# Kernel tuning notes

Measured on AMD Instinct MI355X. Metric: run time of the kernel, lower is better.

## Reference

```python
import jax, jax.numpy as jnp
import numpy as np

IMAGE_SIZE = 256
NEAR = 0.1
FAR = 100.0
EPS = 1e-3
BACKGROUND = jnp.array([0.0, 0.0, 0.0], dtype=jnp.float32)
CHUNK = 64  # faces processed per scan step (keeps [B,CHUNK,3,P] intermediate ~100MB)


def setup_inputs() -> dict:
    key = jax.random.key(0)
    k1, k2, k3, k4 = jax.random.split(key, 4)
    B, F, T = 2, 4096, 4
    # small triangles in NDC with z in (near, far)
    centers = jax.random.uniform(k1, (B, F, 1, 2), minval=-1.0, maxval=1.0)
    offsets = 0.15 * jax.random.normal(k2, (B, F, 3, 2))
    xy = centers + offsets
    z = jax.random.uniform(k3, (B, F, 1, 1), minval=1.0, maxval=20.0) \
        + 0.1 * jax.random.normal(k4, (B, F, 3, 1))
    faces = jnp.concatenate([xy, z], axis=-1).astype(jnp.float32)  # [B,F,3,3]
    textures = jax.random.uniform(jax.random.fold_in(key, 7), (B, F, T, T, T, 3),
                                  dtype=jnp.float32)
    return {"faces": faces, "textures": textures}


def _pixel_grid(is_):
    c = (2.0 * jnp.arange(is_, dtype=jnp.float32) + 1.0 - is_) / is_
    # kernel iterates rows top->bottom with y flipped (y up in NDC)
    yp, xp = jnp.meshgrid(-c, c, indexing="ij")  # [H,W]
    return xp.reshape(-1), yp.reshape(-1)  # [P]


def _raster_chunk(fchunk, xp, yp, near, far):
    # fchunk: [B,C,3verts,3coords]; xp,yp: [P]
    x = fchunk[..., 0]
    y = fchunk[..., 1]
    z = fchunk[..., 2]  # [B,C,3]
    x0, x1, x2 = x[..., 0:1], x[..., 1:2], x[..., 2:3]
    y0, y1, y2 = y[..., 0:1], y[..., 1:2], y[..., 2:3]

    # inside test: pixel on the CCW side of all 3 edges (back faces culled)
    def edge(ya, xa, yb, xb):
        return (yp - ya) * (xb - xa) - (xp - xa) * (yb - ya)  # [B,C,P]
    inside = (edge(y0, x0, y1, x1) >= 0) & (edge(y1, x1, y2, x2) >= 0) \
             & (edge(y2, x2, y0, x0) >= 0)

    # inverse of [[x0,y0,1],[x1,y1,1],[x2,y2,1]] via adjugate (as in CUDA kernel)
    x0s, x1s, x2s = x[..., 0], x[..., 1], x[..., 2]
    y0s, y1s, y2s = y[..., 0], y[..., 1], y[..., 2]
    det = x2s * (y0s - y1s) + x0s * (y1s - y2s) + x1s * (y2s - y0s)
    det = jnp.where(det >= 0, jnp.maximum(det, 1e-10), jnp.minimum(det, -1e-10))
    inv = jnp.stack([
        jnp.stack([y1s - y2s, x2s - x1s, x1s * y2s - x2s * y1s], -1),
        jnp.stack([y2s - y0s, x0s - x2s, x2s * y0s - x0s * y2s], -1),
        jnp.stack([y0s - y1s, x1s - x0s, x0s * y1s - x1s * y0s], -1),
    ], -2) / det[..., None, None]  # [B,C,3,3]

    # barycentric weights per pixel: [B,C,3,P]
    w = inv[..., 0, None] * xp + inv[..., 1, None] * yp + inv[..., 2, None]
    w = jnp.clip(w, 0.0, 1.0)
    w = w / jnp.maximum(w.sum(axis=2, keepdims=True), 1e-10)

    # perspective-correct depth: 1/zp = sum_k w_k / z_k
    inv_zp = (w / z[..., None]).sum(axis=2)  # [B,C,P]
    zp = 1.0 / jnp.maximum(inv_zp, 1e-10)
    valid = inside & (zp > near) & (zp < far)
    zp = jnp.where(valid, zp, far)
    return zp, jnp.moveaxis(w, 2, 3)  # zp:[B,C,P], w:[B,C,P,3]


def _rasterize_maps(faces, image_size, near, far):
    B, F = faces.shape[:2]
    P = image_size * image_size
    xp, yp = _pixel_grid(image_size)
    n_chunks = F // CHUNK
    fch = faces.reshape(B, n_chunks, CHUNK, 3, 3).transpose(1, 0, 2, 3, 4)
    ids = jnp.arange(F, dtype=jnp.int32).reshape(n_chunks, CHUNK)
    init = (jnp.full((B, P), far, jnp.float32),        # best depth (z-buffer)
            jnp.full((B, P), -1, jnp.int32),            # best face index
            jnp.zeros((B, P, 3), jnp.float32))          # best barycentric weights

    def step(carry, inp):
        bz, bf, bw = carry
        fchunk, idc = inp
        zp, w = _raster_chunk(fchunk, xp, yp, near, far)
        am = jnp.argmin(zp, axis=1)  # [B,P] nearest face within chunk
        zmin = jnp.take_along_axis(zp, am[:, None, :], axis=1)[:, 0]          # [B,P]
        wsel = jnp.take_along_axis(w, am[:, None, :, None], axis=1)[:, 0]     # [B,P,3]
        fsel = idc[am]                                                        # [B,P]
        upd = zmin < bz
        return (jnp.where(upd, zmin, bz),
                jnp.where(upd, fsel, bf),
                jnp.where(upd[..., None], wsel, bw)), None

    (bz, bf, bw), _ = jax.lax.scan(jax.checkpoint(step), init, (fch, ids))
    return bf, bw, bz  # face_index_map, weight_map, depth_map (flat pixels)


def _forward(faces, textures):
    B, F = faces.shape[:2]
    T = textures.shape[2]
    is_ = IMAGE_SIZE
    P = is_ * is_
    fidx, w, zp = _rasterize_maps(faces, is_, NEAR, FAR)
    mask = fidx >= 0
    fi = jnp.maximum(fidx, 0)

    # per-pixel vertex depths of hit face: [B,P,3]
    faces_z = faces[..., 2]
    fz = jax.vmap(lambda a, i: a[i])(faces_z, fi)

    # texture cube coords with perspective correction (as in CUDA kernel)
    tif = jnp.clip(w * (T - 1) * (zp[..., None] / fz), 0.0, T - 1 - EPS)
    lo = jnp.floor(tif).astype(jnp.int32)
    frac = tif - lo

    tex_flat = textures.reshape(B, F, T * T * T, 3)
    rgb = jnp.zeros((B, P, 3), jnp.float32)
    for pn in range(8):  # trilinear blend over 8 cube corners
        bits = [(pn >> k) & 1 for k in range(3)]
        idx = lo + jnp.array(bits, jnp.int32)
        wc = jnp.ones_like(frac[..., 0])
        for k in range(3):
            wc = wc * (frac[..., k] if bits[k] else (1.0 - frac[..., k]))
        lin = (idx[..., 0] * T + idx[..., 1]) * T + idx[..., 2]
        texel = jax.vmap(lambda tf, f, l: tf[f, l])(tex_flat, fi, lin)  # [B,P,3]
        rgb = rgb + wc[..., None] * texel

    rgb = jnp.where(mask[..., None], rgb, BACKGROUND)
    alpha = mask.astype(jnp.float32)
    return (rgb.reshape(B, is_, is_, 3),
            alpha.reshape(B, is_, is_),
            zp.reshape(B, is_, is_))


def reference(faces, textures):
    return _forward(faces, textures)
```

## Files before the change

kernel.cpp:

```cpp
#include <hip/hip_runtime.h>

#define IS 256
#define FNUM 4096
#define BATCH 2
#define NSPLIT 16
#define FSPLIT (FNUM / NSPLIT)
#define FAR_ 100.0f
#define NEAR_ 0.1f


__global__ __launch_bounds__(256, 8) void raster_kernel(
    const float* __restrict__ faces, unsigned int* __restrict__ keys)
{
#pragma clang fp contract(off)
  __shared__ float rec[256 * 12];
  __shared__ int cnt[4];

  const int tid = threadIdx.x;
  const int wid = tid >> 6, lane = tid & 63;
  const int z = blockIdx.z;
  const int b = z >> 4;
  const int split = z & 15;

  const int qx = tid & 15, qy = tid >> 4;
  const int col0 = blockIdx.x * 32 + qx * 2;
  const int row0 = blockIdx.y * 32 + qy * 2;

  const float xpA = (2.0f * (float)col0 + 1.0f - 256.0f) * (1.0f / 256.0f);
  const float xpB = (2.0f * (float)(col0 + 1) + 1.0f - 256.0f) * (1.0f / 256.0f);
  const float ypA = -((2.0f * (float)row0 + 1.0f - 256.0f) * (1.0f / 256.0f));
  const float ypB = -((2.0f * (float)(row0 + 1) + 1.0f - 256.0f) * (1.0f / 256.0f));

  const float txmin = (2.0f * (float)(blockIdx.x * 32) + 1.0f - 256.0f) * (1.0f / 256.0f) - 1e-3f;
  const float txmax = (2.0f * (float)(blockIdx.x * 32 + 31) + 1.0f - 256.0f) * (1.0f / 256.0f) + 1e-3f;
  const float tymax = -((2.0f * (float)(blockIdx.y * 32) + 1.0f - 256.0f) * (1.0f / 256.0f)) + 1e-3f;
  const float tymin = -((2.0f * (float)(blockIdx.y * 32 + 31) + 1.0f - 256.0f) * (1.0f / 256.0f)) - 1e-3f;

  const int f = split * FSPLIT + tid;
  const float* fp = faces + ((size_t)b * FNUM + f) * 9;
  const float x0 = fp[0], y0 = fp[1], z0 = fp[2];
  const float x1 = fp[3], y1 = fp[4], z1 = fp[5];
  const float x2 = fp[6], y2 = fp[7], z2 = fp[8];

  const float det = x2 * (y0 - y1) + x0 * (y1 - y2) + x1 * (y2 - y0);
  const float minx = fminf(fminf(x0, x1), x2), maxx = fmaxf(fmaxf(x0, x1), x2);
  const float miny = fminf(fminf(y0, y1), y2), maxy = fmaxf(fmaxf(y0, y1), y2);
  const bool keep = (det >= -1e-5f) &&
                    (minx <= txmax) && (maxx >= txmin) &&
                    (miny <= tymax) && (maxy >= tymin);

  const unsigned long long m = __ballot(keep);
  if (lane == 0) cnt[wid] = __popcll(m);
  __syncthreads();
  const int total = cnt[0] + cnt[1] + cnt[2] + cnt[3];
  if (keep) {
    int base = 0;
    for (int w = 0; w < wid; ++w) base += cnt[w];
    const int pos = base + __popcll(m & ((1ull << lane) - 1ull));
    const float cd = (det >= 0.0f) ? fmaxf(det, 1e-10f) : fminf(det, -1e-10f);
    const float rdet = __builtin_amdgcn_rcpf(cd);
    const float u0 = __builtin_amdgcn_rcpf(z0) * rdet;
    const float u1 = __builtin_amdgcn_rcpf(z1) * rdet;
    const float u2 = __builtin_amdgcn_rcpf(z2) * rdet;
    float4* r4 = (float4*)&rec[pos * 12];
    r4[0] = make_float4(x0, y0, x1, y1);
    r4[1] = make_float4(x2, y2, u0, u1);
    r4[2] = make_float4(u2, __int_as_float(f), 0.0f, 0.0f);
  }
  __syncthreads();

  unsigned int kAA = ~0u, kAB = ~0u, kBA = ~0u, kBB = ~0u;
  for (int i = 0; i < total; ++i) {
    const float4 r0 = ((const float4*)rec)[i * 3 + 0];
    const float4 r1 = ((const float4*)rec)[i * 3 + 1];
    const float4 r2 = ((const float4*)rec)[i * 3 + 2];
    const float fx0 = r0.x, fy0 = r0.y, fx1 = r0.z, fy1 = r0.w;
    const float fx2 = r1.x, fy2 = r1.y, u0 = r1.z, u1 = r1.w;
    const float u2 = r2.x;
    const unsigned int fid = (unsigned int)__float_as_int(r2.y);

    const float t01x = fx1 - fx0, t01y = fy1 - fy0;
    const float t12x = fx2 - fx1, t12y = fy2 - fy1;
    const float t20x = fx0 - fx2, t20y = fy0 - fy2;

    const float a01A = (ypA - fy0) * t01x, a01B = (ypB - fy0) * t01x;
    const float b01A = (xpA - fx0) * t01y, b01B = (xpB - fx0) * t01y;
    const float a12A = (ypA - fy1) * t12x, a12B = (ypB - fy1) * t12x;
    const float b12A = (xpA - fx1) * t12y, b12B = (xpB - fx1) * t12y;
    const float a20A = (ypA - fy2) * t20x, a20B = (ypB - fy2) * t20x;
    const float b20A = (xpA - fx2) * t20y, b20B = (xpB - fx2) * t20y;

#define PX(KK, AR, AC)                                                        \
    {                                                                         \
      const float e01 = a01##AR - b01##AC;                                    \
      const float e12 = a12##AR - b12##AC;                                    \
      const float e20 = a20##AR - b20##AC;                                    \
      const bool inside = fminf(fminf(e01, e12), e20) >= 0.0f;                \
      const float izp = fmaf(e12, u0, fmaf(e20, u1, e01 * u2));               \
      const bool valid = inside && (izp > 0.01f) && (izp < 10.0f);            \
      const unsigned int key =                                                \
          valid ? ((~__float_as_uint(izp)) & 0xFFFFF000u) | fid : ~0u;        \
      KK = (key < KK) ? key : KK;                                             \
    }
    PX(kAA, A, A) PX(kAB, A, B) PX(kBA, B, A) PX(kBB, B, B)
#undef PX
  }

  const int pbase = b * 65536 + row0 * 256 + col0;
  if (kAA != ~0u) atomicMin(&keys[pbase], kAA);
  if (kAB != ~0u) atomicMin(&keys[pbase + 1], kAB);
  if (kBA != ~0u) atomicMin(&keys[pbase + 256], kBA);
  if (kBB != ~0u) atomicMin(&keys[pbase + 257], kBB);
}

struct __attribute__((packed, aligned(4))) F6 { float v[6]; };
struct __attribute__((packed, aligned(4))) F9 { float v[9]; };

__global__ __launch_bounds__(256) void resolve_kernel(
    const float* __restrict__ faces, const float* __restrict__ tex,
    const unsigned int* __restrict__ keys,
    float* __restrict__ out_rgb, float* __restrict__ out_alpha,
    float* __restrict__ out_z)
{
#pragma clang fp contract(off)
  const int p = blockIdx.x * 256 + threadIdx.x;
  const int b = p >> 16;
  const int pi = p & 65535;
  const int row = pi >> 8, col = pi & 255;

  const unsigned int key = keys[p];
  if (key == ~0u) {
    out_rgb[(size_t)p * 3 + 0] = 0.0f;
    out_rgb[(size_t)p * 3 + 1] = 0.0f;
    out_rgb[(size_t)p * 3 + 2] = 0.0f;
    out_alpha[p] = 0.0f;
    out_z[p] = FAR_;
    return;
  }

  const int fid = (int)(key & 0xFFFu);
  const float xp = (2.0f * (float)col + 1.0f - 256.0f) * (1.0f / 256.0f);
  const float yp = -((2.0f * (float)row + 1.0f - 256.0f) * (1.0f / 256.0f));

  const F9 fdat = *(const F9*)(faces + ((size_t)b * FNUM + fid) * 9);
  const float x0 = fdat.v[0], y0 = fdat.v[1], z0 = fdat.v[2];
  const float x1 = fdat.v[3], y1 = fdat.v[4], z1 = fdat.v[5];
  const float x2 = fdat.v[6], y2 = fdat.v[7], z2 = fdat.v[8];

  const float det = x2 * (y0 - y1) + x0 * (y1 - y2) + x1 * (y2 - y0);
  const float cd = (det >= 0.0f) ? fmaxf(det, 1e-10f) : fminf(det, -1e-10f);
  const float rdet = __builtin_amdgcn_rcpf(cd);
  const float rz0 = __builtin_amdgcn_rcpf(z0);
  const float rz1 = __builtin_amdgcn_rcpf(z1);
  const float rz2 = __builtin_amdgcn_rcpf(z2);

  const float e01 = (yp - y0) * (x1 - x0) - (xp - x0) * (y1 - y0);
  const float e12 = (yp - y1) * (x2 - x1) - (xp - x1) * (y2 - y1);
  const float e20 = (yp - y2) * (x0 - x2) - (xp - x2) * (y0 - y2);

  float c0 = fminf(fmaxf(e12 * rdet, 0.0f), 1.0f);
  float c1 = fminf(fmaxf(e20 * rdet, 0.0f), 1.0f);
  float c2 = fminf(fmaxf(e01 * rdet, 0.0f), 1.0f);
  const float s = fmaxf((c0 + c1) + c2, 1e-10f);
  const float rs = __builtin_amdgcn_rcpf(s);
  const float w0 = c0 * rs, w1 = c1 * rs, w2 = c2 * rs;
  const float izp = (w0 * rz0 + w1 * rz1) + w2 * rz2;
  const float zp = __builtin_amdgcn_rcpf(fmaxf(izp, 1e-10f));

  const float t0 = fminf(fmaxf((w0 * 3.0f) * (zp * rz0), 0.0f), 2.999f);
  const float t1 = fminf(fmaxf((w1 * 3.0f) * (zp * rz1), 0.0f), 2.999f);
  const float t2 = fminf(fmaxf((w2 * 3.0f) * (zp * rz2), 0.0f), 2.999f);
  const float l0 = floorf(t0), l1 = floorf(t1), l2 = floorf(t2);
  const int i0 = (int)l0, i1 = (int)l1, i2 = (int)l2;
  const float fr0 = t0 - l0, fr1 = t1 - l1, fr2 = t2 - l2;
  const float g0 = 1.0f - fr0, g1 = 1.0f - fr1, g2 = 1.0f - fr2;

  const float* tb = tex + ((size_t)b * FNUM + fid) * 192;
  float rr = 0.f, rg = 0.f, rb = 0.f;
#pragma unroll
  for (int pn = 0; pn < 4; ++pn) {
    const int b0 = pn & 1, b1 = (pn >> 1) & 1;
    const float w01 = (b0 ? fr0 : g0) * (b1 ? fr1 : g1);
    const float wz0 = w01 * g2, wz1 = w01 * fr2;
    const int lin0 = ((i0 + b0) * 4 + (i1 + b1)) * 4 + i2;
    const F6 t6 = *(const F6*)(tb + lin0 * 3);
    rr = rr + wz0 * t6.v[0] + wz1 * t6.v[3];
    rg = rg + wz0 * t6.v[1] + wz1 * t6.v[4];
    rb = rb + wz0 * t6.v[2] + wz1 * t6.v[5];
  }

  out_rgb[(size_t)p * 3 + 0] = rr;
  out_rgb[(size_t)p * 3 + 1] = rg;
  out_rgb[(size_t)p * 3 + 2] = rb;
  out_alpha[p] = 1.0f;
  out_z[p] = zp;
}

extern "C" void kernel_launch(void* const* d_in, const int* in_sizes, int n_in,
                              void* d_out, int out_size, void* d_ws, size_t ws_size,
                              hipStream_t stream) {
  const float* faces = (const float*)d_in[0];
  const float* tex   = (const float*)d_in[1];
  float* out = (float*)d_out;
  float* out_rgb   = out;
  float* out_alpha = out + 393216;
  float* out_z     = out + 393216 + 131072;

  unsigned int* keys = (unsigned int*)d_ws;
  hipMemsetAsync(keys, 0xFF, (size_t)BATCH * IS * IS * sizeof(unsigned int), stream);

  dim3 gridA(IS / 32, IS / 32, BATCH * NSPLIT);
  hipLaunchKernelGGL(raster_kernel, gridA, dim3(256), 0, stream, faces, keys);

  dim3 gridC((BATCH * IS * IS) / 256, 1, 1);
  hipLaunchKernelGGL(resolve_kernel, gridC, dim3(256), 0, stream,
                     faces, tex, keys, out_rgb, out_alpha, out_z);
}
```

Baseline: 75.50 us.

## Fuse resolve pass into raster kernel via last-block-per-tile ticket

Removes the separate resolve kernel. Each raster block increments a per-tile ticket counter, and the last of the split blocks for a tile shades that tile's pixels, reading keys with atomic loads. This saves one kernel launch and the round trip through the global key buffer. In exchange it adds a second memset for the tickets and concentrates the shading on only one block per tile. It also relies on atomics for cross-block visibility without an explicit fence.

```diff
diff --git a/kernel.cpp b/kernel.cpp
--- a/kernel.cpp
+++ b/kernel.cpp
@@ -7,14 +7,19 @@
 #define FSPLIT (FNUM / NSPLIT)
 #define FAR_ 100.0f
 #define NEAR_ 0.1f
+#define NTILE 64
 
 
 __global__ __launch_bounds__(256, 8) void raster_kernel(
-    const float* __restrict__ faces, unsigned int* __restrict__ keys)
+    const float* __restrict__ faces, const float* __restrict__ tex,
+    unsigned int* __restrict__ keys, unsigned int* __restrict__ tickets,
+    float* __restrict__ out_rgb, float* __restrict__ out_alpha,
+    float* __restrict__ out_z)
 {
 #pragma clang fp contract(off)
   __shared__ float rec[256 * 12];
   __shared__ int cnt[4];
+  __shared__ int lastflag;
 
   const int tid = threadIdx.x;
   const int wid = tid >> 6, lane = tid & 63;
@@ -36,38 +41,40 @@
   const float tymax = -((2.0f * (float)(blockIdx.y * 32) + 1.0f - 256.0f) * (1.0f / 256.0f)) + 1e-3f;
   const float tymin = -((2.0f * (float)(blockIdx.y * 32 + 31) + 1.0f - 256.0f) * (1.0f / 256.0f)) - 1e-3f;
 
-  const int f = split * FSPLIT + tid;
-  const float* fp = faces + ((size_t)b * FNUM + f) * 9;
-  const float x0 = fp[0], y0 = fp[1], z0 = fp[2];
-  const float x1 = fp[3], y1 = fp[4], z1 = fp[5];
-  const float x2 = fp[6], y2 = fp[7], z2 = fp[8];
-
-  const float det = x2 * (y0 - y1) + x0 * (y1 - y2) + x1 * (y2 - y0);
-  const float minx = fminf(fminf(x0, x1), x2), maxx = fmaxf(fmaxf(x0, x1), x2);
-  const float miny = fminf(fminf(y0, y1), y2), maxy = fmaxf(fmaxf(y0, y1), y2);
-  const bool keep = (det >= -1e-5f) &&
-                    (minx <= txmax) && (maxx >= txmin) &&
-                    (miny <= tymax) && (maxy >= tymin);
-
-  const unsigned long long m = __ballot(keep);
-  if (lane == 0) cnt[wid] = __popcll(m);
+  {
+    const int f = split * FSPLIT + tid;
+    const float* fp = faces + ((size_t)b * FNUM + f) * 9;
+    const float x0 = fp[0], y0 = fp[1], z0 = fp[2];
+    const float x1 = fp[3], y1 = fp[4], z1 = fp[5];
+    const float x2 = fp[6], y2 = fp[7], z2 = fp[8];
+
+    const float det = x2 * (y0 - y1) + x0 * (y1 - y2) + x1 * (y2 - y0);
+    const float minx = fminf(fminf(x0, x1), x2), maxx = fmaxf(fmaxf(x0, x1), x2);
+    const float miny = fminf(fminf(y0, y1), y2), maxy = fmaxf(fmaxf(y0, y1), y2);
+    const bool keep = (det >= -1e-5f) &&
+                      (minx <= txmax) && (maxx >= txmin) &&
+                      (miny <= tymax) && (maxy >= tymin);
+
+    const unsigned long long m = __ballot(keep);
+    if (lane == 0) cnt[wid] = __popcll(m);
+    __syncthreads();
+    if (keep) {
+      int base = 0;
+      for (int w = 0; w < wid; ++w) base += cnt[w];
+      const int pos = base + __popcll(m & ((1ull << lane) - 1ull));
+      const float cd = (det >= 0.0f) ? fmaxf(det, 1e-10f) : fminf(det, -1e-10f);
+      const float rdet = __builtin_amdgcn_rcpf(cd);
+      const float u0 = __builtin_amdgcn_rcpf(z0) * rdet;
+      const float u1 = __builtin_amdgcn_rcpf(z1) * rdet;
+      const float u2 = __builtin_amdgcn_rcpf(z2) * rdet;
+      float4* r4 = (float4*)&rec[pos * 12];
+      r4[0] = make_float4(x0, y0, x1, y1);
+      r4[1] = make_float4(x2, y2, u0, u1);
+      r4[2] = make_float4(u2, __int_as_float(f), 0.0f, 0.0f);
+    }
+  }
   __syncthreads();
   const int total = cnt[0] + cnt[1] + cnt[2] + cnt[3];
-  if (keep) {
-    int base = 0;
-    for (int w = 0; w < wid; ++w) base += cnt[w];
-    const int pos = base + __popcll(m & ((1ull << lane) - 1ull));
-    const float cd = (det >= 0.0f) ? fmaxf(det, 1e-10f) : fminf(det, -1e-10f);
-    const float rdet = __builtin_amdgcn_rcpf(cd);
-    const float u0 = __builtin_amdgcn_rcpf(z0) * rdet;
-    const float u1 = __builtin_amdgcn_rcpf(z1) * rdet;
-    const float u2 = __builtin_amdgcn_rcpf(z2) * rdet;
-    float4* r4 = (float4*)&rec[pos * 12];
-    r4[0] = make_float4(x0, y0, x1, y1);
-    r4[1] = make_float4(x2, y2, u0, u1);
-    r4[2] = make_float4(u2, __int_as_float(f), 0.0f, 0.0f);
-  }
-  __syncthreads();
 
   unsigned int kAA = ~0u, kAB = ~0u, kBA = ~0u, kBB = ~0u;
   for (int i = 0; i < total; ++i) {
@@ -111,89 +118,89 @@
   if (kAB != ~0u) atomicMin(&keys[pbase + 1], kAB);
   if (kBA != ~0u) atomicMin(&keys[pbase + 256], kBA);
   if (kBB != ~0u) atomicMin(&keys[pbase + 257], kBB);
-}
-
-struct __attribute__((packed, aligned(4))) F6 { float v[6]; };
-struct __attribute__((packed, aligned(4))) F9 { float v[9]; };
-
-__global__ __launch_bounds__(256) void resolve_kernel(
-    const float* __restrict__ faces, const float* __restrict__ tex,
-    const unsigned int* __restrict__ keys,
-    float* __restrict__ out_rgb, float* __restrict__ out_alpha,
-    float* __restrict__ out_z)
-{
-#pragma clang fp contract(off)
-  const int p = blockIdx.x * 256 + threadIdx.x;
-  const int b = p >> 16;
-  const int pi = p & 65535;
-  const int row = pi >> 8, col = pi & 255;
-
-  const unsigned int key = keys[p];
-  if (key == ~0u) {
-    out_rgb[(size_t)p * 3 + 0] = 0.0f;
-    out_rgb[(size_t)p * 3 + 1] = 0.0f;
-    out_rgb[(size_t)p * 3 + 2] = 0.0f;
-    out_alpha[p] = 0.0f;
-    out_z[p] = FAR_;
-    return;
-  }
-
-  const int fid = (int)(key & 0xFFFu);
-  const float xp = (2.0f * (float)col + 1.0f - 256.0f) * (1.0f / 256.0f);
-  const float yp = -((2.0f * (float)row + 1.0f - 256.0f) * (1.0f / 256.0f));
-
-  const F9 fdat = *(const F9*)(faces + ((size_t)b * FNUM + fid) * 9);
-  const float x0 = fdat.v[0], y0 = fdat.v[1], z0 = fdat.v[2];
-  const float x1 = fdat.v[3], y1 = fdat.v[4], z1 = fdat.v[5];
-  const float x2 = fdat.v[6], y2 = fdat.v[7], z2 = fdat.v[8];
-
-  const float det = x2 * (y0 - y1) + x0 * (y1 - y2) + x1 * (y2 - y0);
-  const float cd = (det >= 0.0f) ? fmaxf(det, 1e-10f) : fminf(det, -1e-10f);
-  const float rdet = __builtin_amdgcn_rcpf(cd);
-  const float rz0 = __builtin_amdgcn_rcpf(z0);
-  const float rz1 = __builtin_amdgcn_rcpf(z1);
-  const float rz2 = __builtin_amdgcn_rcpf(z2);
-
-  const float e01 = (yp - y0) * (x1 - x0) - (xp - x0) * (y1 - y0);
-  const float e12 = (yp - y1) * (x2 - x1) - (xp - x1) * (y2 - y1);
-  const float e20 = (yp - y2) * (x0 - x2) - (xp - x2) * (y0 - y2);
-
-  float c0 = fminf(fmaxf(e12 * rdet, 0.0f), 1.0f);
-  float c1 = fminf(fmaxf(e20 * rdet, 0.0f), 1.0f);
-  float c2 = fminf(fmaxf(e01 * rdet, 0.0f), 1.0f);
-  const float s = fmaxf((c0 + c1) + c2, 1e-10f);
-  const float rs = __builtin_amdgcn_rcpf(s);
-  const float w0 = c0 * rs, w1 = c1 * rs, w2 = c2 * rs;
-  const float izp = (w0 * rz0 + w1 * rz1) + w2 * rz2;
-  const float zp = __builtin_amdgcn_rcpf(fmaxf(izp, 1e-10f));
-
-  const float t0 = fminf(fmaxf((w0 * 3.0f) * (zp * rz0), 0.0f), 2.999f);
-  const float t1 = fminf(fmaxf((w1 * 3.0f) * (zp * rz1), 0.0f), 2.999f);
-  const float t2 = fminf(fmaxf((w2 * 3.0f) * (zp * rz2), 0.0f), 2.999f);
-  const float l0 = floorf(t0), l1 = floorf(t1), l2 = floorf(t2);
-  const int i0 = (int)l0, i1 = (int)l1, i2 = (int)l2;
-  const float fr0 = t0 - l0, fr1 = t1 - l1, fr2 = t2 - l2;
-  const float g0 = 1.0f - fr0, g1 = 1.0f - fr1, g2 = 1.0f - fr2;
-
-  const float* tb = tex + ((size_t)b * FNUM + fid) * 192;
-  float rr = 0.f, rg = 0.f, rb = 0.f;
+
+  __syncthreads();
+  const int tileId = b * NTILE + (int)blockIdx.y * 8 + (int)blockIdx.x;
+  if (tid == 0) {
+    const unsigned int t = atomicAdd(&tickets[tileId], 1u);
+    lastflag = (t == NSPLIT - 1);
+  }
+  __syncthreads();
+  if (!lastflag) return;
+
+  for (int q = 0; q < 4; ++q) {
+    const int row = row0 + (q >> 1);
+    const int col = col0 + (q & 1);
+    const int p = b * 65536 + row * 256 + col;
+
+    const unsigned int key = atomicMin(&keys[p], ~0u);
+
+    if (key == ~0u) {
+      out_rgb[(size_t)p * 3 + 0] = 0.0f;
+      out_rgb[(size_t)p * 3 + 1] = 0.0f;
+      out_rgb[(size_t)p * 3 + 2] = 0.0f;
+      out_alpha[p] = 0.0f;
+      out_z[p] = FAR_;
+      continue;
+    }
+
+    const int fid = (int)(key & 0xFFFu);
+    const float xp = (2.0f * (float)col + 1.0f - 256.0f) * (1.0f / 256.0f);
+    const float yp = -((2.0f * (float)row + 1.0f - 256.0f) * (1.0f / 256.0f));
+
+    const float* fp = faces + ((size_t)b * FNUM + fid) * 9;
+    const float x0 = fp[0], y0 = fp[1], z0 = fp[2];
+    const float x1 = fp[3], y1 = fp[4], z1 = fp[5];
+    const float x2 = fp[6], y2 = fp[7], z2 = fp[8];
+
+    const float det = x2 * (y0 - y1) + x0 * (y1 - y2) + x1 * (y2 - y0);
+    const float cd = (det >= 0.0f) ? fmaxf(det, 1e-10f) : fminf(det, -1e-10f);
+    const float rdet = __builtin_amdgcn_rcpf(cd);
+    const float rz0 = __builtin_amdgcn_rcpf(z0);
+    const float rz1 = __builtin_amdgcn_rcpf(z1);
+    const float rz2 = __builtin_amdgcn_rcpf(z2);
+
+    const float e01 = (yp - y0) * (x1 - x0) - (xp - x0) * (y1 - y0);
+    const float e12 = (yp - y1) * (x2 - x1) - (xp - x1) * (y2 - y1);
+    const float e20 = (yp - y2) * (x0 - x2) - (xp - x2) * (y0 - y2);
+
+    const float c0 = fminf(fmaxf(e12 * rdet, 0.0f), 1.0f);
+    const float c1 = fminf(fmaxf(e20 * rdet, 0.0f), 1.0f);
+    const float c2 = fminf(fmaxf(e01 * rdet, 0.0f), 1.0f);
+    const float s = fmaxf((c0 + c1) + c2, 1e-10f);
+    const float rs = __builtin_amdgcn_rcpf(s);
+    const float w0 = c0 * rs, w1 = c1 * rs, w2 = c2 * rs;
+    const float izp = (w0 * rz0 + w1 * rz1) + w2 * rz2;
+    const float zp = __builtin_amdgcn_rcpf(fmaxf(izp, 1e-10f));
+
+    const float t0 = fminf(fmaxf((w0 * 3.0f) * (zp * rz0), 0.0f), 2.999f);
+    const float t1 = fminf(fmaxf((w1 * 3.0f) * (zp * rz1), 0.0f), 2.999f);
+    const float t2 = fminf(fmaxf((w2 * 3.0f) * (zp * rz2), 0.0f), 2.999f);
+    const float l0 = floorf(t0), l1 = floorf(t1), l2 = floorf(t2);
+    const int i0 = (int)l0, i1 = (int)l1, i2 = (int)l2;
+    const float fr0 = t0 - l0, fr1 = t1 - l1, fr2 = t2 - l2;
+    const float g0 = 1.0f - fr0, g1 = 1.0f - fr1, g2 = 1.0f - fr2;
+
+    const float* tb = tex + ((size_t)b * FNUM + fid) * 192;
+    float rr = 0.f, rg = 0.f, rb = 0.f;
 #pragma unroll
-  for (int pn = 0; pn < 4; ++pn) {
-    const int b0 = pn & 1, b1 = (pn >> 1) & 1;
-    const float w01 = (b0 ? fr0 : g0) * (b1 ? fr1 : g1);
-    const float wz0 = w01 * g2, wz1 = w01 * fr2;
-    const int lin0 = ((i0 + b0) * 4 + (i1 + b1)) * 4 + i2;
-    const F6 t6 = *(const F6*)(tb + lin0 * 3);
-    rr = rr + wz0 * t6.v[0] + wz1 * t6.v[3];
-    rg = rg + wz0 * t6.v[1] + wz1 * t6.v[4];
-    rb = rb + wz0 * t6.v[2] + wz1 * t6.v[5];
-  }
-
-  out_rgb[(size_t)p * 3 + 0] = rr;
-  out_rgb[(size_t)p * 3 + 1] = rg;
-  out_rgb[(size_t)p * 3 + 2] = rb;
-  out_alpha[p] = 1.0f;
-  out_z[p] = zp;
+    for (int pn = 0; pn < 4; ++pn) {
+      const int b0 = pn & 1, b1 = (pn >> 1) & 1;
+      const float w01 = (b0 ? fr0 : g0) * (b1 ? fr1 : g1);
+      const float wz0 = w01 * g2, wz1 = w01 * fr2;
+      const int lin0 = ((i0 + b0) * 4 + (i1 + b1)) * 4 + i2;
+      const float* tp = tb + lin0 * 3;
+      rr = rr + wz0 * tp[0] + wz1 * tp[3];
+      rg = rg + wz0 * tp[1] + wz1 * tp[4];
+      rb = rb + wz0 * tp[2] + wz1 * tp[5];
+    }
+
+    out_rgb[(size_t)p * 3 + 0] = rr;
+    out_rgb[(size_t)p * 3 + 1] = rg;
+    out_rgb[(size_t)p * 3 + 2] = rb;
+    out_alpha[p] = 1.0f;
+    out_z[p] = zp;
+  }
 }
 
 extern "C" void kernel_launch(void* const* d_in, const int* in_sizes, int n_in,
@@ -206,13 +213,12 @@
   float* out_alpha = out + 393216;
   float* out_z     = out + 393216 + 131072;
 
-  unsigned int* keys = (unsigned int*)d_ws;
-  hipMemsetAsync(keys, 0xFF, (size_t)BATCH * IS * IS * sizeof(unsigned int), stream);
+  unsigned int* keys    = (unsigned int*)d_ws;
+  unsigned int* tickets = keys + BATCH * IS * IS;
+  hipMemsetAsync(keys, 0xFF, ((size_t)BATCH * IS * IS) * 4, stream);
+  hipMemsetAsync(tickets, 0x00, (size_t)BATCH * NTILE * 4, stream);
 
   dim3 gridA(IS / 32, IS / 32, BATCH * NSPLIT);
-  hipLaunchKernelGGL(raster_kernel, gridA, dim3(256), 0, stream, faces, keys);
-
-  dim3 gridC((BATCH * IS * IS) / 256, 1, 1);
-  hipLaunchKernelGGL(resolve_kernel, gridC, dim3(256), 0, stream,
-                     faces, tex, keys, out_rgb, out_alpha, out_z);
+  hipLaunchKernelGGL(raster_kernel, gridA, dim3(256), 0, stream,
+                     faces, tex, keys, tickets, out_rgb, out_alpha, out_z);
 }
```

Result: slower. 81.00 us (+7.3%).
